# Optimization experiments

Measured on AMD Instinct MI355X. Metric: run time of the kernel, lower is better.

## Reference

```python
import jax, jax.numpy as jnp
import numpy as np


def conv2d(x, w, stride=1, padding=0):
    # x: [N,Ci,H,W], w: [Co,Ci,Kh,Kw]
    return jax.lax.conv_general_dilated(
        x, w, window_strides=(stride, stride),
        padding=[(padding, padding), (padding, padding)],
        dimension_numbers=('NCHW', 'OIHW', 'NCHW'))


def adder2d(x, w, stride=1, padding=0):
    """AdderNet L1-distance conv: out[n,co,ho,wo] = -sum_{ci,kh,kw} |x_patch - w[co,ci,kh,kw]|."""
    N, Ci, H, W = x.shape
    Co, _, K, _ = w.shape
    xp = jnp.pad(x, ((0, 0), (0, 0), (padding, padding), (padding, padding)))
    Ho = (H + 2 * padding - K) // stride + 1
    Wo = (W + 2 * padding - K) // stride + 1
    acc = jnp.zeros((N, Co, Ho, Wo), x.dtype)
    for kh in range(K):  # small fixed loop over kernel taps (<=9)
        for kw in range(K):
            xs = xp[:, :, kh:kh + Ho * stride:stride, kw:kw + Wo * stride:stride]  # [N,Ci,Ho,Wo]
            diff = jnp.abs(xs[:, None] - w[None, :, :, kh, kw, None, None])  # [N,Co,Ci,Ho,Wo]
            acc = acc - diff.sum(axis=2)
    return acc


def batchnorm(x, gamma, beta, mean, var, eps=1e-5):
    inv = gamma / jnp.sqrt(var + eps)
    return x * inv[None, :, None, None] + (beta - mean * inv)[None, :, None, None]


def setup_inputs() -> dict:
    key = jax.random.key(0)
    ks = jax.random.split(key, 16)
    N, C, H, W = 4, 128, 28, 28
    inp = {
        'x': jax.random.normal(ks[0], (N, C, H, W), jnp.float32),
        'w_shift1': jax.random.normal(ks[1], (C, C, 1, 1), jnp.float32) * 0.1,
        'w_add1': jax.random.normal(ks[2], (C, C, 1, 1), jnp.float32) * 0.1,
        'bn1_gamma': jax.random.uniform(ks[3], (C,), jnp.float32, 0.5, 1.5),
        'bn1_beta': jax.random.normal(ks[4], (C,), jnp.float32) * 0.1,
        'bn1_mean': jax.random.normal(ks[5], (C,), jnp.float32),
        'bn1_var': jax.random.uniform(ks[6], (C,), jnp.float32, 0.5, 1.5),
        'w_shift2': jax.random.normal(ks[7], (C, C, 3, 3), jnp.float32) * 0.05,
        'w_add2': jax.random.normal(ks[8], (C, C, 3, 3), jnp.float32) * 0.05,
        'bn2_gamma': jax.random.uniform(ks[9], (C,), jnp.float32, 0.5, 1.5),
        'bn2_beta': jax.random.normal(ks[10], (C,), jnp.float32) * 0.1,
        'bn2_mean': jax.random.normal(ks[11], (C,), jnp.float32),
        'bn2_var': jax.random.uniform(ks[12], (C,), jnp.float32, 0.5, 1.5),
    }
    return inp


def reference(x, w_shift1, w_add1, bn1_gamma, bn1_beta, bn1_mean, bn1_var,
              w_shift2, w_add2, bn2_gamma, bn2_beta, bn2_mean, bn2_var):
    identity = x
    # conv1: 1x1 shift conv -> 1x1 adder
    out = conv2d(x, w_shift1, stride=1, padding=0)
    out = adder2d(out, w_add1, stride=1, padding=0)
    out = jax.nn.relu(batchnorm(out, bn1_gamma, bn1_beta, bn1_mean, bn1_var))
    # conv2: 3x3 shift conv (stride=1, pad=1) -> 3x3 adder (stride=1, pad=1)
    out = conv2d(out, w_shift2, stride=1, padding=1)
    out = adder2d(out, w_add2, stride=1, padding=1)
    out = jax.nn.relu(batchnorm(out, bn2_gamma, bn2_beta, bn2_mean, bn2_var))
    return jax.nn.relu(out + identity)
```

## Files before the change

kernel.cpp:

```cpp
#include <hip/hip_runtime.h>
#include <math.h>

constexpr int C   = 128;
constexpr int HW  = 784;
constexpr int PW  = 30;
constexpr int PHW = 900;

#define ABS_ACC(acc, d) asm("v_add_f32 %0, %0, abs(%1)" : "+v"(acc) : "v"(d))

__device__ inline void tile_map(int wg, int& n, int& h0, int& w0) {
    int region = wg & 7;
    int idx    = wg >> 3;
    n = region >> 1;
    int half = region & 1;
    int th = half * 7 + idx / 14;
    int tw = idx % 14;
    h0 = th * 2;
    w0 = tw * 2;
}

__device__ inline void zero_border(float* plane, int h0, int w0) {
    if (h0 == 0) {
        plane[w0 + 1] = 0.f; plane[w0 + 2] = 0.f;
        if (w0 == 0)  plane[0]  = 0.f;
        if (w0 == 26) plane[29] = 0.f;
    }
    if (h0 == 26) {
        plane[29 * PW + w0 + 1] = 0.f; plane[29 * PW + w0 + 2] = 0.f;
        if (w0 == 0)  plane[29 * PW]      = 0.f;
        if (w0 == 26) plane[29 * PW + 29] = 0.f;
    }
    if (w0 == 0)  { plane[(h0 + 1) * PW]      = 0.f; plane[(h0 + 2) * PW]      = 0.f; }
    if (w0 == 26) { plane[(h0 + 1) * PW + 29] = 0.f; plane[(h0 + 2) * PW + 29] = 0.f; }
}

__global__ __launch_bounds__(256) void reorder_w(const float* __restrict__ w2,
                                                 const float* __restrict__ a2,
                                                 const float* __restrict__ w1,
                                                 const float* __restrict__ a1,
                                                 float* __restrict__ w2r,
                                                 float* __restrict__ a2r,
                                                 float* __restrict__ w1r,
                                                 float* __restrict__ a1r) {
    int idx = blockIdx.x * 256 + threadIdx.x;
    const int T9 = C * C * 9;
    const int T1 = C * C;
    if (idx < 2 * T9) {
        const float* src = w2; float* dst = w2r;
        if (idx >= T9) { idx -= T9; src = a2; dst = a2r; }
        int co = idx & 127;
        int r  = idx >> 7;
        int k  = r % 9;
        int ci = r / 9;
        dst[idx] = src[(co * C + ci) * 9 + k];
        return;
    }
    idx -= 2 * T9;
    if (idx >= 2 * T1) return;
    const float* src = w1; float* dst = w1r;
    if (idx >= T1) { idx -= T1; src = a1; dst = a1r; }
    int co = idx & 127;
    int ci = idx >> 7;
    dst[idx] = src[co * C + ci];
}

__global__ __launch_bounds__(256, 8) void stage1(const float* __restrict__ x,
                                                 const float* __restrict__ w1r,
                                                 const float* __restrict__ a1r,
                                                 const float* __restrict__ g1,
                                                 const float* __restrict__ b1,
                                                 const float* __restrict__ m1,
                                                 const float* __restrict__ v1,
                                                 float* __restrict__ t1p) {
    __shared__ float Xs[C][4];
    __shared__ float Ys[C][4];
    __shared__ float Rs[C][4];
    int n, h0, w0;
    tile_map(blockIdx.x, n, h0, w0);
    int t   = threadIdx.x;
    int co  = t & 127;
    int ciq = t >> 7;
    int ci0 = ciq * 64;

#pragma unroll
    for (int e = t; e < 512; e += 256) {
        int ci = e >> 2, p = e & 3, r = p >> 1, c = p & 1;
        Xs[ci][p] = x[(n * C + ci) * HW + (h0 + r) * 28 + w0 + c];
    }
    __syncthreads();

    float4 a = make_float4(0.f, 0.f, 0.f, 0.f);
    const float* wp = w1r + co;
#pragma unroll 4
    for (int i = 0; i < 64; ++i) {
        int ci = ci0 + i;
        float wv = wp[ci * C];
        float4 xv = *reinterpret_cast<const float4*>(&Xs[ci][0]);
        a.x = fmaf(xv.x, wv, a.x);
        a.y = fmaf(xv.y, wv, a.y);
        a.z = fmaf(xv.z, wv, a.z);
        a.w = fmaf(xv.w, wv, a.w);
    }
    if (ciq) *reinterpret_cast<float4*>(&Rs[co][0]) = a;
    __syncthreads();
    if (ciq == 0) {
        float4 r = *reinterpret_cast<const float4*>(&Rs[co][0]);
        a.x += r.x; a.y += r.y; a.z += r.z; a.w += r.w;
        *reinterpret_cast<float4*>(&Ys[co][0]) = a;
    }
    __syncthreads();

    float d0 = 0.f, d1 = 0.f, d2 = 0.f, d3 = 0.f;
    const float* ap = a1r + co;
#pragma unroll 4
    for (int i = 0; i < 64; ++i) {
        int ci = ci0 + i;
        float av = ap[ci * C];
        float4 yv = *reinterpret_cast<const float4*>(&Ys[ci][0]);
        float e0 = yv.x - av; ABS_ACC(d0, e0);
        float e1 = yv.y - av; ABS_ACC(d1, e1);
        float e2 = yv.z - av; ABS_ACC(d2, e2);
        float e3 = yv.w - av; ABS_ACC(d3, e3);
    }
    if (ciq) *reinterpret_cast<float4*>(&Rs[co][0]) = make_float4(d0, d1, d2, d3);
    __syncthreads();
    if (ciq == 0) {
        float4 r = *reinterpret_cast<const float4*>(&Rs[co][0]);
        d0 += r.x; d1 += r.y; d2 += r.z; d3 += r.w;
        float inv = g1[co] / sqrtf(v1[co] + 1e-5f);
        float off = b1[co] - m1[co] * inv;
        float* plane = t1p + (n * C + co) * PHW;
        float* dst = plane + (h0 + 1) * PW + (w0 + 1);
        dst[0]      = fmaxf(-d0 * inv + off, 0.f);
        dst[1]      = fmaxf(-d1 * inv + off, 0.f);
        dst[PW + 0] = fmaxf(-d2 * inv + off, 0.f);
        dst[PW + 1] = fmaxf(-d3 * inv + off, 0.f);
        zero_border(plane, h0, w0);
    }
}

__global__ __launch_bounds__(256, 8) void conv3x3(const float* __restrict__ t1p,
                                                  const float* __restrict__ w2r,
                                                  float* __restrict__ t2p) {
    __shared__ float Rs[C][4];
    int n, h0, w0;
    tile_map(blockIdx.x, n, h0, w0);
    int t   = threadIdx.x;
    int co  = t & 127;
    int ciq = t >> 7;
    int ci0u = __builtin_amdgcn_readfirstlane(ciq * 64);

    const float* sp0 = t1p + n * C * PHW + h0 * PW + w0;
    const float* wb  = w2r + co;
    float acc[4] = {0.f, 0.f, 0.f, 0.f};

#pragma unroll 2
    for (int i = 0; i < 64; ++i) {
        int ci = ci0u + i;
        const float* wp = wb + ci * 9 * C;
        float wk[9];
#pragma unroll
        for (int k = 0; k < 9; ++k) wk[k] = wp[k * C];
        const float* sp = sp0 + ci * PHW;
        float xr[4][4];
#pragma unroll
        for (int r = 0; r < 4; ++r)
#pragma unroll
            for (int c = 0; c < 4; ++c) xr[r][c] = sp[r * PW + c];
#pragma unroll
        for (int kh = 0; kh < 3; ++kh)
#pragma unroll
            for (int kw = 0; kw < 3; ++kw) {
                float wv = wk[kh * 3 + kw];
                acc[0] = fmaf(xr[kh + 0][kw + 0], wv, acc[0]);
                acc[1] = fmaf(xr[kh + 0][kw + 1], wv, acc[1]);
                acc[2] = fmaf(xr[kh + 1][kw + 0], wv, acc[2]);
                acc[3] = fmaf(xr[kh + 1][kw + 1], wv, acc[3]);
            }
    }
    if (ciq) *reinterpret_cast<float4*>(&Rs[co][0]) = make_float4(acc[0], acc[1], acc[2], acc[3]);
    __syncthreads();
    if (ciq == 0) {
        float4 r = *reinterpret_cast<const float4*>(&Rs[co][0]);
        acc[0] += r.x; acc[1] += r.y; acc[2] += r.z; acc[3] += r.w;
        float* plane = t2p + (n * C + co) * PHW;
        float* dst = plane + (h0 + 1) * PW + (w0 + 1);
        dst[0]      = acc[0];
        dst[1]      = acc[1];
        dst[PW + 0] = acc[2];
        dst[PW + 1] = acc[3];
        zero_border(plane, h0, w0);
    }
}

__global__ __launch_bounds__(256, 8) void adder3x3(const float* __restrict__ t2p,
                                                   const float* __restrict__ a2r,
                                                   const float* __restrict__ x0,
                                                   const float* __restrict__ g2,
                                                   const float* __restrict__ b2,
                                                   const float* __restrict__ m2,
                                                   const float* __restrict__ v2,
                                                   float* __restrict__ out) {
    __shared__ float Rs[C][4];
    int n, h0, w0;
    tile_map(blockIdx.x, n, h0, w0);
    int t   = threadIdx.x;
    int co  = t & 127;
    int ciq = t >> 7;
    int ci0u = __builtin_amdgcn_readfirstlane(ciq * 64);

    const float* sp0 = t2p + n * C * PHW + h0 * PW + w0;
    const float* ab  = a2r + co;
    float acc[4] = {0.f, 0.f, 0.f, 0.f};

#pragma unroll 2
    for (int i = 0; i < 64; ++i) {
        int ci = ci0u + i;
        const float* wp = ab + ci * 9 * C;
        float wk[9];
#pragma unroll
        for (int k = 0; k < 9; ++k) wk[k] = wp[k * C];
        const float* sp = sp0 + ci * PHW;
        float xr[4][4];
#pragma unroll
        for (int r = 0; r < 4; ++r)
#pragma unroll
            for (int c = 0; c < 4; ++c) xr[r][c] = sp[r * PW + c];
#pragma unroll
        for (int kh = 0; kh < 3; ++kh)
#pragma unroll
            for (int kw = 0; kw < 3; ++kw) {
                float wv = wk[kh * 3 + kw];
                float e0 = xr[kh + 0][kw + 0] - wv; ABS_ACC(acc[0], e0);
                float e1 = xr[kh + 0][kw + 1] - wv; ABS_ACC(acc[1], e1);
                float e2 = xr[kh + 1][kw + 0] - wv; ABS_ACC(acc[2], e2);
                float e3 = xr[kh + 1][kw + 1] - wv; ABS_ACC(acc[3], e3);
            }
    }
    if (ciq) *reinterpret_cast<float4*>(&Rs[co][0]) = make_float4(acc[0], acc[1], acc[2], acc[3]);
    __syncthreads();
    if (ciq == 0) {
        float4 r = *reinterpret_cast<const float4*>(&Rs[co][0]);
        acc[0] += r.x; acc[1] += r.y; acc[2] += r.z; acc[3] += r.w;
        float inv = g2[co] / sqrtf(v2[co] + 1e-5f);
        float off = b2[co] - m2[co] * inv;
        int base = (n * C + co) * HW + h0 * 28 + w0;
        float z0 = fmaxf(-acc[0] * inv + off, 0.f) + x0[base + 0];
        float z1 = fmaxf(-acc[1] * inv + off, 0.f) + x0[base + 1];
        float z2 = fmaxf(-acc[2] * inv + off, 0.f) + x0[base + 28];
        float z3 = fmaxf(-acc[3] * inv + off, 0.f) + x0[base + 29];
        out[base + 0]  = fmaxf(z0, 0.f);
        out[base + 1]  = fmaxf(z1, 0.f);
        out[base + 28] = fmaxf(z2, 0.f);
        out[base + 29] = fmaxf(z3, 0.f);
    }
}

extern "C" void kernel_launch(void* const* d_in, const int* in_sizes, int n_in,
                              void* d_out, int out_size, void* d_ws, size_t ws_size,
                              hipStream_t stream) {
    const float* x   = (const float*)d_in[0];
    const float* w1  = (const float*)d_in[1];
    const float* a1  = (const float*)d_in[2];
    const float* g1  = (const float*)d_in[3];
    const float* b1  = (const float*)d_in[4];
    const float* m1  = (const float*)d_in[5];
    const float* v1  = (const float*)d_in[6];
    const float* w2  = (const float*)d_in[7];
    const float* a2  = (const float*)d_in[8];
    const float* g2  = (const float*)d_in[9];
    const float* b2  = (const float*)d_in[10];
    const float* m2  = (const float*)d_in[11];
    const float* v2  = (const float*)d_in[12];
    float* out = (float*)d_out;

    float* ws  = (float*)d_ws;
    float* t1p = ws;
    float* t2p = t1p + 4 * C * PHW;
    float* w2r = t2p + 4 * C * PHW;
    float* a2r = w2r + C * C * 9;
    float* w1r = a2r + C * C * 9;
    float* a1r = w1r + C * C;

    const int reorder_total = 2 * C * C * 9 + 2 * C * C;
    reorder_w<<<(reorder_total + 255) / 256, 256, 0, stream>>>(w2, a2, w1, a1, w2r, a2r, w1r, a1r);
    stage1<<<784, 256, 0, stream>>>(x, w1r, a1r, g1, b1, m1, v1, t1p);
    conv3x3<<<784, 256, 0, stream>>>(t1p, w2r, t2p);
    adder3x3<<<784, 256, 0, stream>>>(t2p, a2r, x, g2, b2, m2, v2, out);
}
```

Baseline: 80.65 us.

## Widen 3x3 conv/adder tiles to 2x4 pixels with 64-channel output split

The 3x3 shift-conv and adder kernels now compute a 2x4 output tile per thread over 64 output channels, splitting the input channels four ways (32 each) instead of two ways. Each loaded 4x6 input patch and the 9 weights are reused across 8 outputs instead of 4, which lowers loads per arithmetic op. The workgroup count stays the same because the output channels are split in half. The cost is more registers per thread and a larger shared-memory reduction across the four input-channel groups.

Result: faster. 69.37 us (-14.0%).

```diff
diff --git a/kernel.cpp b/kernel.cpp
--- a/kernel.cpp
+++ b/kernel.cpp
@@ -8,7 +8,7 @@
 
 #define ABS_ACC(acc, d) asm("v_add_f32 %0, %0, abs(%1)" : "+v"(acc) : "v"(d))
 
-__device__ inline void tile_map(int wg, int& n, int& h0, int& w0) {
+__device__ inline void tile_map2(int wg, int& n, int& h0, int& w0) {
     int region = wg & 7;
     int idx    = wg >> 3;
     n = region >> 1;
@@ -19,7 +19,19 @@
     w0 = tw * 2;
 }
 
-__device__ inline void zero_border(float* plane, int h0, int w0) {
+__device__ inline void tile_map4(int wg, int& n, int& h0, int& w0, int& co0) {
+    int region = wg & 7;
+    int rest   = wg >> 3;
+    n = region >> 1;
+    int half = region & 1;
+    co0 = (rest & 1) * 64;
+    int idx = rest >> 1;
+    int th = idx / 7, tw = idx % 7;
+    h0 = half * 14 + th * 2;
+    w0 = tw * 4;
+}
+
+__device__ inline void zero_border2(float* plane, int h0, int w0) {
     if (h0 == 0) {
         plane[w0 + 1] = 0.f; plane[w0 + 2] = 0.f;
         if (w0 == 0)  plane[0]  = 0.f;
@@ -32,6 +44,23 @@
     }
     if (w0 == 0)  { plane[(h0 + 1) * PW]      = 0.f; plane[(h0 + 2) * PW]      = 0.f; }
     if (w0 == 26) { plane[(h0 + 1) * PW + 29] = 0.f; plane[(h0 + 2) * PW + 29] = 0.f; }
+}
+
+__device__ inline void zero_border4(float* plane, int h0, int w0) {
+    if (h0 == 0) {
+#pragma unroll
+        for (int c = 0; c < 4; ++c) plane[w0 + 1 + c] = 0.f;
+        if (w0 == 0)  plane[0]  = 0.f;
+        if (w0 == 24) plane[29] = 0.f;
+    }
+    if (h0 == 26) {
+#pragma unroll
+        for (int c = 0; c < 4; ++c) plane[29 * PW + w0 + 1 + c] = 0.f;
+        if (w0 == 0)  plane[29 * PW]      = 0.f;
+        if (w0 == 24) plane[29 * PW + 29] = 0.f;
+    }
+    if (w0 == 0)  { plane[(h0 + 1) * PW]      = 0.f; plane[(h0 + 2) * PW]      = 0.f; }
+    if (w0 == 24) { plane[(h0 + 1) * PW + 29] = 0.f; plane[(h0 + 2) * PW + 29] = 0.f; }
 }
 
 __global__ __launch_bounds__(256) void reorder_w(const float* __restrict__ w2,
@@ -76,7 +105,7 @@
     __shared__ float Ys[C][4];
     __shared__ float Rs[C][4];
     int n, h0, w0;
-    tile_map(blockIdx.x, n, h0, w0);
+    tile_map2(blockIdx.x, n, h0, w0);
     int t   = threadIdx.x;
     int co  = t & 127;
     int ciq = t >> 7;
@@ -135,61 +164,71 @@
         dst[1]      = fmaxf(-d1 * inv + off, 0.f);
         dst[PW + 0] = fmaxf(-d2 * inv + off, 0.f);
         dst[PW + 1] = fmaxf(-d3 * inv + off, 0.f);
-        zero_border(plane, h0, w0);
+        zero_border2(plane, h0, w0);
     }
 }
 
 __global__ __launch_bounds__(256, 8) void conv3x3(const float* __restrict__ t1p,
                                                   const float* __restrict__ w2r,
                                                   float* __restrict__ t2p) {
-    __shared__ float Rs[C][4];
-    int n, h0, w0;
-    tile_map(blockIdx.x, n, h0, w0);
+    __shared__ float Rs[3][64][8];
+    int n, h0, w0, co0;
+    tile_map4(blockIdx.x, n, h0, w0, co0);
     int t   = threadIdx.x;
-    int co  = t & 127;
-    int ciq = t >> 7;
-    int ci0u = __builtin_amdgcn_readfirstlane(ciq * 64);
+    int col = t & 63;
+    int co  = co0 + col;
+    int ciq = t >> 6;
+    int ci0u = __builtin_amdgcn_readfirstlane(ciq * 32);
 
     const float* sp0 = t1p + n * C * PHW + h0 * PW + w0;
     const float* wb  = w2r + co;
-    float acc[4] = {0.f, 0.f, 0.f, 0.f};
+    float acc[2][4] = {{0.f,0.f,0.f,0.f},{0.f,0.f,0.f,0.f}};
 
 #pragma unroll 2
-    for (int i = 0; i < 64; ++i) {
+    for (int i = 0; i < 32; ++i) {
         int ci = ci0u + i;
         const float* wp = wb + ci * 9 * C;
         float wk[9];
 #pragma unroll
         for (int k = 0; k < 9; ++k) wk[k] = wp[k * C];
         const float* sp = sp0 + ci * PHW;
-        float xr[4][4];
+        float xr[4][6];
 #pragma unroll
         for (int r = 0; r < 4; ++r)
 #pragma unroll
-            for (int c = 0; c < 4; ++c) xr[r][c] = sp[r * PW + c];
+            for (int c = 0; c < 6; ++c) xr[r][c] = sp[r * PW + c];
 #pragma unroll
         for (int kh = 0; kh < 3; ++kh)
 #pragma unroll
             for (int kw = 0; kw < 3; ++kw) {
                 float wv = wk[kh * 3 + kw];
-                acc[0] = fmaf(xr[kh + 0][kw + 0], wv, acc[0]);
-                acc[1] = fmaf(xr[kh + 0][kw + 1], wv, acc[1]);
-                acc[2] = fmaf(xr[kh + 1][kw + 0], wv, acc[2]);
-                acc[3] = fmaf(xr[kh + 1][kw + 1], wv, acc[3]);
+#pragma unroll
+                for (int pr = 0; pr < 2; ++pr)
+#pragma unroll
+                    for (int pc = 0; pc < 4; ++pc)
+                        acc[pr][pc] = fmaf(xr[pr + kh][pc + kw], wv, acc[pr][pc]);
             }
     }
-    if (ciq) *reinterpret_cast<float4*>(&Rs[co][0]) = make_float4(acc[0], acc[1], acc[2], acc[3]);
+    if (ciq) {
+        *reinterpret_cast<float4*>(&Rs[ciq - 1][col][0]) = make_float4(acc[0][0], acc[0][1], acc[0][2], acc[0][3]);
+        *reinterpret_cast<float4*>(&Rs[ciq - 1][col][4]) = make_float4(acc[1][0], acc[1][1], acc[1][2], acc[1][3]);
+    }
     __syncthreads();
     if (ciq == 0) {
-        float4 r = *reinterpret_cast<const float4*>(&Rs[co][0]);
-        acc[0] += r.x; acc[1] += r.y; acc[2] += r.z; acc[3] += r.w;
+#pragma unroll
+        for (int q = 0; q < 3; ++q) {
+            float4 r0 = *reinterpret_cast<const float4*>(&Rs[q][col][0]);
+            float4 r1 = *reinterpret_cast<const float4*>(&Rs[q][col][4]);
+            acc[0][0] += r0.x; acc[0][1] += r0.y; acc[0][2] += r0.z; acc[0][3] += r0.w;
+            acc[1][0] += r1.x; acc[1][1] += r1.y; acc[1][2] += r1.z; acc[1][3] += r1.w;
+        }
         float* plane = t2p + (n * C + co) * PHW;
         float* dst = plane + (h0 + 1) * PW + (w0 + 1);
-        dst[0]      = acc[0];
-        dst[1]      = acc[1];
-        dst[PW + 0] = acc[2];
-        dst[PW + 1] = acc[3];
-        zero_border(plane, h0, w0);
+#pragma unroll
+        for (int pc = 0; pc < 4; ++pc) dst[pc]      = acc[0][pc];
+#pragma unroll
+        for (int pc = 0; pc < 4; ++pc) dst[PW + pc] = acc[1][pc];
+        zero_border4(plane, h0, w0);
     }
 }
 
@@ -201,58 +240,71 @@
                                                    const float* __restrict__ m2,
                                                    const float* __restrict__ v2,
                                                    float* __restrict__ out) {
-    __shared__ float Rs[C][4];
-    int n, h0, w0;
-    tile_map(blockIdx.x, n, h0, w0);
+    __shared__ float Rs[3][64][8];
+    int n, h0, w0, co0;
+    tile_map4(blockIdx.x, n, h0, w0, co0);
     int t   = threadIdx.x;
-    int co  = t & 127;
-    int ciq = t >> 7;
-    int ci0u = __builtin_amdgcn_readfirstlane(ciq * 64);
+    int col = t & 63;
+    int co  = co0 + col;
+    int ciq = t >> 6;
+    int ci0u = __builtin_amdgcn_readfirstlane(ciq * 32);
 
     const float* sp0 = t2p + n * C * PHW + h0 * PW + w0;
     const float* ab  = a2r + co;
-    float acc[4] = {0.f, 0.f, 0.f, 0.f};
+    float acc[2][4] = {{0.f,0.f,0.f,0.f},{0.f,0.f,0.f,0.f}};
 
 #pragma unroll 2
-    for (int i = 0; i < 64; ++i) {
+    for (int i = 0; i < 32; ++i) {
         int ci = ci0u + i;
         const float* wp = ab + ci * 9 * C;
         float wk[9];
 #pragma unroll
         for (int k = 0; k < 9; ++k) wk[k] = wp[k * C];
         const float* sp = sp0 + ci * PHW;
-        float xr[4][4];
+        float xr[4][6];
 #pragma unroll
         for (int r = 0; r < 4; ++r)
 #pragma unroll
-            for (int c = 0; c < 4; ++c) xr[r][c] = sp[r * PW + c];
+            for (int c = 0; c < 6; ++c) xr[r][c] = sp[r * PW + c];
 #pragma unroll
         for (int kh = 0; kh < 3; ++kh)
 #pragma unroll
             for (int kw = 0; kw < 3; ++kw) {
                 float wv = wk[kh * 3 + kw];
-                float e0 = xr[kh + 0][kw + 0] - wv; ABS_ACC(acc[0], e0);
-                float e1 = xr[kh + 0][kw + 1] - wv; ABS_ACC(acc[1], e1);
-                float e2 = xr[kh + 1][kw + 0] - wv; ABS_ACC(acc[2], e2);
-                float e3 = xr[kh + 1][kw + 1] - wv; ABS_ACC(acc[3], e3);
+#pragma unroll
+                for (int pr = 0; pr < 2; ++pr)
+#pragma unroll
+                    for (int pc = 0; pc < 4; ++pc) {
+                        float e = xr[pr + kh][pc + kw] - wv;
+                        ABS_ACC(acc[pr][pc], e);
+                    }
             }
     }
-    if (ciq) *reinterpret_cast<float4*>(&Rs[co][0]) = make_float4(acc[0], acc[1], acc[2], acc[3]);
+    if (ciq) {
+        *reinterpret_cast<float4*>(&Rs[ciq - 1][col][0]) = make_float4(acc[0][0], acc[0][1], acc[0][2], acc[0][3]);
+        *reinterpret_cast<float4*>(&Rs[ciq - 1][col][4]) = make_float4(acc[1][0], acc[1][1], acc[1][2], acc[1][3]);
+    }
     __syncthreads();
     if (ciq == 0) {
-        float4 r = *reinterpret_cast<const float4*>(&Rs[co][0]);
-        acc[0] += r.x; acc[1] += r.y; acc[2] += r.z; acc[3] += r.w;
+#pragma unroll
+        for (int q = 0; q < 3; ++q) {
+            float4 r0 = *reinterpret_cast<const float4*>(&Rs[q][col][0]);
+            float4 r1 = *reinterpret_cast<const float4*>(&Rs[q][col][4]);
+            acc[0][0] += r0.x; acc[0][1] += r0.y; acc[0][2] += r0.z; acc[0][3] += r0.w;
+            acc[1][0] += r1.x; acc[1][1] += r1.y; acc[1][2] += r1.z; acc[1][3] += r1.w;
+        }
         float inv = g2[co] / sqrtf(v2[co] + 1e-5f);
         float off = b2[co] - m2[co] * inv;
         int base = (n * C + co) * HW + h0 * 28 + w0;
-        float z0 = fmaxf(-acc[0] * inv + off, 0.f) + x0[base + 0];
-        float z1 = fmaxf(-acc[1] * inv + off, 0.f) + x0[base + 1];
-        float z2 = fmaxf(-acc[2] * inv + off, 0.f) + x0[base + 28];
-        float z3 = fmaxf(-acc[3] * inv + off, 0.f) + x0[base + 29];
-        out[base + 0]  = fmaxf(z0, 0.f);
-        out[base + 1]  = fmaxf(z1, 0.f);
-        out[base + 28] = fmaxf(z2, 0.f);
-        out[base + 29] = fmaxf(z3, 0.f);
+#pragma unroll
+        for (int pr = 0; pr < 2; ++pr) {
+#pragma unroll
+            for (int pc = 0; pc < 4; ++pc) {
+                float z = fmaxf(-acc[pr][pc] * inv + off, 0.f);
+                z += x0[base + pr * 28 + pc];
+                out[base + pr * 28 + pc] = fmaxf(z, 0.f);
+            }
+        }
     }
 }
 
```

## Split 3x3 kernels over output-channel halves with 4-way ci split and padded rows

Applied to the files above, without the earlier changes.

The 3x3 conv and adder kernels now launch 1568 workgroups, each covering 64 output channels with four wavefronts splitting the input channels into quarters, reduced through a three-slot shared buffer. The padded plane row pitch grows from 30 to 32 so input rows can be read with float2 loads. The intent is more parallelism and shorter per-thread loops to improve latency hiding. The cost is a larger reduction step and a bigger workspace footprint. Each spatial tile's input is now loaded by two workgroups, one per channel half.

Measured after the change: 73.34 us. 9.1% less time.

```diff
diff --git a/kernel.cpp b/kernel.cpp
--- a/kernel.cpp
+++ b/kernel.cpp
@@ -3,12 +3,13 @@
 
 constexpr int C   = 128;
 constexpr int HW  = 784;
-constexpr int PW  = 30;
-constexpr int PHW = 900;
+constexpr int PW  = 32;
+constexpr int PH  = 30;
+constexpr int PHW = PW * PH;
 
 #define ABS_ACC(acc, d) asm("v_add_f32 %0, %0, abs(%1)" : "+v"(acc) : "v"(d))
 
-__device__ inline void tile_map(int wg, int& n, int& h0, int& w0) {
+__device__ inline void tile_map2(int wg, int& n, int& h0, int& w0) {
     int region = wg & 7;
     int idx    = wg >> 3;
     n = region >> 1;
@@ -19,7 +20,17 @@
     w0 = tw * 2;
 }
 
-__device__ inline void zero_border(float* plane, int h0, int w0) {
+__device__ inline void tile_map22(int wg, int& n, int& h0, int& w0, int& co0) {
+    int region = wg & 7;
+    int idx    = wg >> 3;
+    n   = region >> 1;
+    co0 = (region & 1) * 64;
+    int th = idx / 14, tw = idx % 14;
+    h0 = th * 2;
+    w0 = tw * 2;
+}
+
+__device__ inline void zero_border2(float* plane, int h0, int w0) {
     if (h0 == 0) {
         plane[w0 + 1] = 0.f; plane[w0 + 2] = 0.f;
         if (w0 == 0)  plane[0]  = 0.f;
@@ -76,7 +87,7 @@
     __shared__ float Ys[C][4];
     __shared__ float Rs[C][4];
     int n, h0, w0;
-    tile_map(blockIdx.x, n, h0, w0);
+    tile_map2(blockIdx.x, n, h0, w0);
     int t   = threadIdx.x;
     int co  = t & 127;
     int ciq = t >> 7;
@@ -135,27 +146,28 @@
         dst[1]      = fmaxf(-d1 * inv + off, 0.f);
         dst[PW + 0] = fmaxf(-d2 * inv + off, 0.f);
         dst[PW + 1] = fmaxf(-d3 * inv + off, 0.f);
-        zero_border(plane, h0, w0);
+        zero_border2(plane, h0, w0);
     }
 }
 
 __global__ __launch_bounds__(256, 8) void conv3x3(const float* __restrict__ t1p,
                                                   const float* __restrict__ w2r,
                                                   float* __restrict__ t2p) {
-    __shared__ float Rs[C][4];
-    int n, h0, w0;
-    tile_map(blockIdx.x, n, h0, w0);
+    __shared__ float Rs[3][64][4];
+    int n, h0, w0, co0;
+    tile_map22(blockIdx.x, n, h0, w0, co0);
     int t   = threadIdx.x;
-    int co  = t & 127;
-    int ciq = t >> 7;
-    int ci0u = __builtin_amdgcn_readfirstlane(ciq * 64);
+    int col = t & 63;
+    int co  = co0 + col;
+    int ciq = t >> 6;
+    int ci0u = __builtin_amdgcn_readfirstlane(ciq * 32);
 
     const float* sp0 = t1p + n * C * PHW + h0 * PW + w0;
     const float* wb  = w2r + co;
     float acc[4] = {0.f, 0.f, 0.f, 0.f};
 
-#pragma unroll 2
-    for (int i = 0; i < 64; ++i) {
+#pragma unroll 4
+    for (int i = 0; i < 32; ++i) {
         int ci = ci0u + i;
         const float* wp = wb + ci * 9 * C;
         float wk[9];
@@ -164,9 +176,11 @@
         const float* sp = sp0 + ci * PHW;
         float xr[4][4];
 #pragma unroll
-        for (int r = 0; r < 4; ++r)
-#pragma unroll
-            for (int c = 0; c < 4; ++c) xr[r][c] = sp[r * PW + c];
+        for (int r = 0; r < 4; ++r) {
+            float2 q0 = *reinterpret_cast<const float2*>(sp + r * PW);
+            float2 q1 = *reinterpret_cast<const float2*>(sp + r * PW + 2);
+            xr[r][0] = q0.x; xr[r][1] = q0.y; xr[r][2] = q1.x; xr[r][3] = q1.y;
+        }
 #pragma unroll
         for (int kh = 0; kh < 3; ++kh)
 #pragma unroll
@@ -178,18 +192,22 @@
                 acc[3] = fmaf(xr[kh + 1][kw + 1], wv, acc[3]);
             }
     }
-    if (ciq) *reinterpret_cast<float4*>(&Rs[co][0]) = make_float4(acc[0], acc[1], acc[2], acc[3]);
+    if (ciq) *reinterpret_cast<float4*>(&Rs[ciq - 1][col][0]) =
+        make_float4(acc[0], acc[1], acc[2], acc[3]);
     __syncthreads();
     if (ciq == 0) {
-        float4 r = *reinterpret_cast<const float4*>(&Rs[co][0]);
-        acc[0] += r.x; acc[1] += r.y; acc[2] += r.z; acc[3] += r.w;
+#pragma unroll
+        for (int q = 0; q < 3; ++q) {
+            float4 r = *reinterpret_cast<const float4*>(&Rs[q][col][0]);
+            acc[0] += r.x; acc[1] += r.y; acc[2] += r.z; acc[3] += r.w;
+        }
         float* plane = t2p + (n * C + co) * PHW;
         float* dst = plane + (h0 + 1) * PW + (w0 + 1);
         dst[0]      = acc[0];
         dst[1]      = acc[1];
         dst[PW + 0] = acc[2];
         dst[PW + 1] = acc[3];
-        zero_border(plane, h0, w0);
+        zero_border2(plane, h0, w0);
     }
 }
 
@@ -201,20 +219,21 @@
                                                    const float* __restrict__ m2,
                                                    const float* __restrict__ v2,
                                                    float* __restrict__ out) {
-    __shared__ float Rs[C][4];
-    int n, h0, w0;
-    tile_map(blockIdx.x, n, h0, w0);
+    __shared__ float Rs[3][64][4];
+    int n, h0, w0, co0;
+    tile_map22(blockIdx.x, n, h0, w0, co0);
     int t   = threadIdx.x;
-    int co  = t & 127;
-    int ciq = t >> 7;
-    int ci0u = __builtin_amdgcn_readfirstlane(ciq * 64);
+    int col = t & 63;
+    int co  = co0 + col;
+    int ciq = t >> 6;
+    int ci0u = __builtin_amdgcn_readfirstlane(ciq * 32);
 
     const float* sp0 = t2p + n * C * PHW + h0 * PW + w0;
     const float* ab  = a2r + co;
     float acc[4] = {0.f, 0.f, 0.f, 0.f};
 
-#pragma unroll 2
-    for (int i = 0; i < 64; ++i) {
+#pragma unroll 4
+    for (int i = 0; i < 32; ++i) {
         int ci = ci0u + i;
         const float* wp = ab + ci * 9 * C;
         float wk[9];
@@ -223,9 +242,11 @@
         const float* sp = sp0 + ci * PHW;
         float xr[4][4];
 #pragma unroll
-        for (int r = 0; r < 4; ++r)
-#pragma unroll
-            for (int c = 0; c < 4; ++c) xr[r][c] = sp[r * PW + c];
+        for (int r = 0; r < 4; ++r) {
+            float2 q0 = *reinterpret_cast<const float2*>(sp + r * PW);
+            float2 q1 = *reinterpret_cast<const float2*>(sp + r * PW + 2);
+            xr[r][0] = q0.x; xr[r][1] = q0.y; xr[r][2] = q1.x; xr[r][3] = q1.y;
+        }
 #pragma unroll
         for (int kh = 0; kh < 3; ++kh)
 #pragma unroll
@@ -237,11 +258,15 @@
                 float e3 = xr[kh + 1][kw + 1] - wv; ABS_ACC(acc[3], e3);
             }
     }
-    if (ciq) *reinterpret_cast<float4*>(&Rs[co][0]) = make_float4(acc[0], acc[1], acc[2], acc[3]);
+    if (ciq) *reinterpret_cast<float4*>(&Rs[ciq - 1][col][0]) =
+        make_float4(acc[0], acc[1], acc[2], acc[3]);
     __syncthreads();
     if (ciq == 0) {
-        float4 r = *reinterpret_cast<const float4*>(&Rs[co][0]);
-        acc[0] += r.x; acc[1] += r.y; acc[2] += r.z; acc[3] += r.w;
+#pragma unroll
+        for (int q = 0; q < 3; ++q) {
+            float4 r = *reinterpret_cast<const float4*>(&Rs[q][col][0]);
+            acc[0] += r.x; acc[1] += r.y; acc[2] += r.z; acc[3] += r.w;
+        }
         float inv = g2[co] / sqrtf(v2[co] + 1e-5f);
         float off = b2[co] - m2[co] * inv;
         int base = (n * C + co) * HW + h0 * 28 + w0;
@@ -285,6 +310,6 @@
     const int reorder_total = 2 * C * C * 9 + 2 * C * C;
     reorder_w<<<(reorder_total + 255) / 256, 256, 0, stream>>>(w2, a2, w1, a1, w2r, a2r, w1r, a1r);
     stage1<<<784, 256, 0, stream>>>(x, w1r, a1r, g1, b1, m1, v1, t1p);
-    conv3x3<<<784, 256, 0, stream>>>(t1p, w2r, t2p);
-    adder3x3<<<784, 256, 0, stream>>>(t2p, a2r, x, g2, b2, m2, v2, out);
-}
+    conv3x3<<<1568, 256, 0, stream>>>(t1p, w2r, t2p);
+    adder3x3<<<1568, 256, 0, stream>>>(t2p, a2r, x, g2, b2, m2, v2, out);
+}
```
